# Kernel tuning notes

Measured on AMD Instinct MI355X. Metric: run time of the kernel, lower is better.

The kernel has to match this reference:

```python
import jax, jax.numpy as jnp
import numpy as np

WIN = 64
SHIFT = 32
HEADS = 12


def setup_inputs() -> dict:
    key = jax.random.key(0)
    ks = jax.random.split(key, 6)
    D = 768
    return {
        'x': jax.random.normal(ks[0], (16, 4096, D), dtype=jnp.float32),
        'qkv_w': jax.random.normal(ks[1], (3 * D, D), dtype=jnp.float32) * (D ** -0.5),
        'qkv_b': jax.random.normal(ks[2], (3 * D,), dtype=jnp.float32) * 0.02,
        'proj_w': jax.random.normal(ks[3], (D, D), dtype=jnp.float32) * (D ** -0.5),
        'proj_b': jax.random.normal(ks[4], (D,), dtype=jnp.float32) * 0.02,
        'rel_bias': jax.random.normal(ks[5], (HEADS, 2 * WIN - 1), dtype=jnp.float32) * 0.02,
    }


def reference(x, qkv_w, qkv_b, proj_w, proj_b, rel_bias):
    B, N, D = x.shape
    H, hd = HEADS, D // HEADS
    scale = hd ** -0.5
    if SHIFT:
        x = jnp.roll(x, SHIFT, axis=1)
    pad = (-N) % WIN
    if pad:
        x = jnp.pad(x, ((0, 0), (0, pad), (0, 0)))
    Np = x.shape[1]
    nW = Np // WIN
    # [B*nW, w, D] windows
    xw = x.reshape(B * nW, WIN, D)
    qkv = xw @ qkv_w.T + qkv_b                       # [B*nW, w, 3D]
    qkv = qkv.reshape(B * nW, WIN, 3, H, hd).transpose(2, 0, 3, 1, 4)
    q, k, v = qkv[0], qkv[1], qkv[2]                 # [B*nW, H, w, hd]
    attn = jnp.einsum('bhqd,bhkd->bhqk', q, k) * scale
    idx = jnp.arange(WIN)
    rel = idx[None, :] - idx[:, None] + (WIN - 1)    # [w, w] in [0, 2w-2]
    attn = attn + rel_bias[:, rel][None]             # gather bias per head
    attn = jax.nn.softmax(attn, axis=-1)
    y = jnp.einsum('bhqk,bhkd->bhqd', attn, v)       # [B*nW, H, w, hd]
    y = y.transpose(0, 2, 1, 3).reshape(B * nW, WIN, D)
    y = y @ proj_w.T + proj_b
    y = y.reshape(B, Np, D)
    if pad:
        y = y[:, :N, :]
    if SHIFT:
        y = jnp.roll(y, -SHIFT, axis=1)
    return y
```

## Files before the change

### kernel.cpp

```cpp
#include <hip/hip_runtime.h>
#include <hip/hip_bf16.h>
#include <stdint.h>

#define SEQ     4096
#define NBATCH  16
#define DMODEL  768
#define NHEAD   12
#define HDIM    64
#define WINSZ   64
#define SHIFT_T 32
#define QKV_N   (3*DMODEL)

typedef __attribute__((ext_vector_type(8))) short  bf16x8;
typedef __attribute__((ext_vector_type(4))) float  f32x4;

static __device__ __forceinline__ unsigned short f2bf(float f) {
  union { float f; unsigned u; } v; v.f = f;
  unsigned r = v.u + 0x7fffu + ((v.u >> 16) & 1u);
  return (unsigned short)(r >> 16);
}

__global__ void k_cvt_x(const float* __restrict__ x, unsigned short* __restrict__ xb,
                        long long c0, long long n8) {
  for (long long i = (long long)blockIdx.x*blockDim.x + threadIdx.x; i < n8;
       i += (long long)gridDim.x*blockDim.x) {
    long long e = i*8;
    int d = (int)(e % DMODEL);
    long long gt = c0 + e / DMODEL;
    int t = (int)(gt & (SEQ-1));
    long long b = gt >> 12;
    int ts = (t - SHIFT_T) & (SEQ-1);
    const float* src = x + (((b << 12) + ts) * (long long)DMODEL + d);
    float4 a0 = *(const float4*)src;
    float4 a1 = *(const float4*)(src + 4);
    bf16x8 o;
    o[0]=(short)f2bf(a0.x); o[1]=(short)f2bf(a0.y); o[2]=(short)f2bf(a0.z); o[3]=(short)f2bf(a0.w);
    o[4]=(short)f2bf(a1.x); o[5]=(short)f2bf(a1.y); o[6]=(short)f2bf(a1.z); o[7]=(short)f2bf(a1.w);
    *(bf16x8*)(xb + e) = o;
  }
}

__global__ void k_cvt_w(const float* __restrict__ w, unsigned short* __restrict__ wb, int n8) {
  int i = blockIdx.x*blockDim.x + threadIdx.x;
  if (i >= n8) return;
  float4 a0 = ((const float4*)w)[2*i];
  float4 a1 = ((const float4*)w)[2*i+1];
  bf16x8 o;
  o[0]=(short)f2bf(a0.x); o[1]=(short)f2bf(a0.y); o[2]=(short)f2bf(a0.z); o[3]=(short)f2bf(a0.w);
  o[4]=(short)f2bf(a1.x); o[5]=(short)f2bf(a1.y); o[6]=(short)f2bf(a1.z); o[7]=(short)f2bf(a1.w);
  ((bf16x8*)wb)[i] = o;
}

template<int MODE>
__global__ __launch_bounds__(256, 2)
void k_gemm_bt(const unsigned short* __restrict__ A, const unsigned short* __restrict__ Bw,
               const float* __restrict__ bias, unsigned short* __restrict__ Cb,
               float* __restrict__ Cf, int M, int N, int K, int nTN, long long c0) {
  __shared__ char sA[128*128];
  __shared__ char sB[128*128];
  int nwg = gridDim.x;
  int cpx = nwg >> 3;
  int wg  = (blockIdx.x & 7) * cpx + (blockIdx.x >> 3);
  int bm = wg / nTN, bn = wg % nTN;
  long long m0 = (long long)bm * 128;
  int n0 = bn * 128;
  int lane = threadIdx.x & 63, wid = threadIdx.x >> 6;
  int wr = wid >> 1, wc = wid & 1;
  int l8 = lane >> 3, lc = lane & 7;

  f32x4 acc[4][4];
  #pragma unroll
  for (int i = 0; i < 4; ++i)
    #pragma unroll
    for (int j = 0; j < 4; ++j) acc[i][j] = (f32x4){0.f,0.f,0.f,0.f};

  for (int kt = 0; kt < K; kt += 64) {
    __syncthreads();
    #pragma unroll
    for (int i = 0; i < 4; ++i) {
      int r   = i*4 + wid;
      int row = r*8 + l8;
      int ch  = lc ^ (row & 7);
      const unsigned short* ga = A  + (m0 + row) * (long long)K + kt + ch*8;
      const unsigned short* gb = Bw + (long long)(n0 + row) * K + kt + ch*8;
      __builtin_amdgcn_global_load_lds((const __attribute__((address_space(1))) unsigned int*)(const void*)ga,
          (__attribute__((address_space(3))) unsigned int*)(void*)(sA + r*1024), 16, 0, 0);
      __builtin_amdgcn_global_load_lds((const __attribute__((address_space(1))) unsigned int*)(const void*)gb,
          (__attribute__((address_space(3))) unsigned int*)(void*)(sB + r*1024), 16, 0, 0);
    }
    __syncthreads();
    #pragma unroll
    for (int kk = 0; kk < 2; ++kk) {
      bf16x8 af[4], bf[4];
      #pragma unroll
      for (int mf = 0; mf < 4; ++mf) {
        int row = wr*64 + mf*16 + (lane & 15);
        int p = row*128 + (kk*32 + (lane >> 4)*8)*2;
        af[mf] = *(const bf16x8*)(sA + (p ^ ((row & 7) << 4)));
      }
      #pragma unroll
      for (int nf = 0; nf < 4; ++nf) {
        int row = wc*64 + nf*16 + (lane & 15);
        int p = row*128 + (kk*32 + (lane >> 4)*8)*2;
        bf[nf] = *(const bf16x8*)(sB + (p ^ ((row & 7) << 4)));
      }
      #pragma unroll
      for (int mf = 0; mf < 4; ++mf)
        #pragma unroll
        for (int nf = 0; nf < 4; ++nf)
          acc[mf][nf] = __builtin_amdgcn_mfma_f32_16x16x32_bf16(af[mf], bf[nf], acc[mf][nf], 0, 0, 0);
    }
  }

  int cl = lane & 15, g4 = lane >> 4;
  #pragma unroll
  for (int mf = 0; mf < 4; ++mf) {
    #pragma unroll
    for (int nf = 0; nf < 4; ++nf) {
      int n = n0 + wc*64 + nf*16 + cl;
      float bv = bias[n];
      #pragma unroll
      for (int r = 0; r < 4; ++r) {
        long long m = m0 + wr*64 + mf*16 + g4*4 + r;
        float v = acc[mf][nf][r] + bv;
        if (MODE == 0) {
          Cb[m * (long long)N + n] = f2bf(v);
        } else {
          long long gm = c0 + m;
          long long om = (gm & ~(long long)(SEQ-1)) | ((gm - SHIFT_T) & (long long)(SEQ-1));
          Cf[om * (long long)N + n] = v;
        }
      }
    }
  }
}

__global__ __launch_bounds__(256, 4)
void k_attn(const unsigned short* __restrict__ qkv, const float* __restrict__ rel_bias,
            unsigned short* __restrict__ y) {
  int w = blockIdx.x / NHEAD;
  int h = blockIdx.x - w*NHEAD;
  __shared__ unsigned short sQ[64*72], sK[64*72], sV[64*72];
  __shared__ unsigned short sP[4][16*72];
  __shared__ float rb[128];
  int tid = threadIdx.x, lane = tid & 63, wid = tid >> 6;
  int cl = lane & 15, g4 = lane >> 4;

  if (tid < 2*WINSZ - 1) rb[tid] = rel_bias[h*(2*WINSZ-1) + tid];

  const unsigned short* base = qkv + (long long)w*WINSZ*QKV_N + h*HDIM;
  #pragma unroll
  for (int pass = 0; pass < 2; ++pass) {
    int row = (tid >> 3) + pass*32;
    int ch  = tid & 7;
    const unsigned short* src = base + (long long)row*QKV_N + ch*8;
    *(bf16x8*)(sQ + row*72 + ch*8) = *(const bf16x8*)(src);
    *(bf16x8*)(sK + row*72 + ch*8) = *(const bf16x8*)(src + DMODEL);
    *(bf16x8*)(sV + row*72 + ch*8) = *(const bf16x8*)(src + 2*DMODEL);
  }
  __syncthreads();

  f32x4 sc[4];
  #pragma unroll
  for (int nt = 0; nt < 4; ++nt) sc[nt] = (f32x4){0.f,0.f,0.f,0.f};
  #pragma unroll
  for (int kk = 0; kk < 2; ++kk) {
    bf16x8 aq = *(const bf16x8*)(sQ + (wid*16 + cl)*72 + kk*32 + g4*8);
    #pragma unroll
    for (int nt = 0; nt < 4; ++nt) {
      bf16x8 bk = *(const bf16x8*)(sK + (nt*16 + cl)*72 + kk*32 + g4*8);
      sc[nt] = __builtin_amdgcn_mfma_f32_16x16x32_bf16(aq, bk, sc[nt], 0, 0, 0);
    }
  }

  float pv[4][4];
  #pragma unroll
  for (int r = 0; r < 4; ++r) {
    int qi = wid*16 + g4*4 + r;
    float mx = -1e30f;
    #pragma unroll
    for (int nt = 0; nt < 4; ++nt) {
      int kj = nt*16 + cl;
      float v = sc[nt][r]*0.125f + rb[kj - qi + (WINSZ-1)];
      pv[nt][r] = v;
      mx = fmaxf(mx, v);
    }
    #pragma unroll
    for (int m = 1; m < 16; m <<= 1) mx = fmaxf(mx, __shfl_xor(mx, m, 64));
    float sum = 0.f;
    #pragma unroll
    for (int nt = 0; nt < 4; ++nt) { float e = __expf(pv[nt][r]-mx); pv[nt][r] = e; sum += e; }
    #pragma unroll
    for (int m = 1; m < 16; m <<= 1) sum += __shfl_xor(sum, m, 64);
    float inv = 1.f / sum;
    #pragma unroll
    for (int nt = 0; nt < 4; ++nt)
      sP[wid][(g4*4+r)*72 + nt*16 + cl] = f2bf(pv[nt][r]*inv);
  }

  f32x4 o[4];
  #pragma unroll
  for (int nt = 0; nt < 4; ++nt) o[nt] = (f32x4){0.f,0.f,0.f,0.f};
  #pragma unroll
  for (int kk = 0; kk < 2; ++kk) {
    bf16x8 ap = *(const bf16x8*)(&sP[wid][cl*72 + kk*32 + g4*8]);
    #pragma unroll
    for (int nt = 0; nt < 4; ++nt) {
      bf16x8 bv;
      #pragma unroll
      for (int j = 0; j < 8; ++j)
        bv[j] = (short)sV[(kk*32 + g4*8 + j)*72 + nt*16 + cl];
      o[nt] = __builtin_amdgcn_mfma_f32_16x16x32_bf16(ap, bv, o[nt], 0, 0, 0);
    }
  }

  long long tokbase = (long long)w * WINSZ;
  #pragma unroll
  for (int nt = 0; nt < 4; ++nt)
    #pragma unroll
    for (int r = 0; r < 4; ++r) {
      int row = wid*16 + g4*4 + r;
      y[(tokbase + row) * (long long)DMODEL + h*HDIM + nt*16 + cl] = f2bf(o[nt][r]);
    }
}

extern "C" void kernel_launch(void* const* d_in, const int* in_sizes, int n_in,
                              void* d_out, int out_size, void* d_ws, size_t ws_size,
                              hipStream_t stream) {
  const float* x      = (const float*)d_in[0];
  const float* qkv_w  = (const float*)d_in[1];
  const float* qkv_b  = (const float*)d_in[2];
  const float* proj_w = (const float*)d_in[3];
  const float* proj_b = (const float*)d_in[4];
  const float* rel_b  = (const float*)d_in[5];
  float* out = (float*)d_out;

  const long long NTOK = (long long)NBATCH * SEQ;
  const size_t wbytes = (size_t)QKV_N*DMODEL*2 + (size_t)DMODEL*DMODEL*2;

  int C = 16;
  for (int c : {1, 2, 4, 8, 16}) {
    size_t tpc = (size_t)NTOK / c;
    size_t need = tpc*QKV_N*2 + tpc*DMODEL*2 + wbytes;
    if (need <= ws_size) { C = c; break; }
  }
  long long tpc = NTOK / C;

  char* ws = (char*)d_ws;
  unsigned short* qkvb = (unsigned short*)ws;
  unsigned short* xb   = (unsigned short*)(ws + (size_t)tpc*QKV_N*2);
  unsigned short* wq   = (unsigned short*)(ws + (size_t)tpc*QKV_N*2 + (size_t)tpc*DMODEL*2);
  unsigned short* wp   = wq + (size_t)QKV_N*DMODEL;

  k_cvt_w<<<(QKV_N*DMODEL/8 + 255)/256, 256, 0, stream>>>(qkv_w, wq, QKV_N*DMODEL/8);
  k_cvt_w<<<(DMODEL*DMODEL/8 + 255)/256, 256, 0, stream>>>(proj_w, wp, DMODEL*DMODEL/8);

  for (int c = 0; c < C; ++c) {
    long long c0 = (long long)c * tpc;
    long long n8 = tpc * DMODEL / 8;
    int cvtGrid = (int)((n8 + 255) / 256); if (cvtGrid > 2048) cvtGrid = 2048;
    k_cvt_x<<<cvtGrid, 256, 0, stream>>>(x, xb, c0, n8);

    int mT = (int)(tpc / 128);
    k_gemm_bt<0><<<mT * (QKV_N/128), 256, 0, stream>>>(xb, wq, qkv_b, qkvb, nullptr,
                                                       (int)tpc, QKV_N, DMODEL, QKV_N/128, c0);
    k_attn<<<(int)(tpc/WINSZ) * NHEAD, 256, 0, stream>>>(qkvb, rel_b, xb );
    k_gemm_bt<1><<<mT * (DMODEL/128), 256, 0, stream>>>(xb, wp, proj_b, nullptr, out,
                                                        (int)tpc, DMODEL, DMODEL, DMODEL/128, c0);
  }
}
```

Measured before the change: 559.9 us.

## Replace GEMM with 256x256-tile, 8-wave, 4-stage LDS-pipelined kernel

```diff
diff --git a/kernel.cpp b/kernel.cpp
--- a/kernel.cpp
+++ b/kernel.cpp
@@ -19,6 +19,10 @@
   unsigned r = v.u + 0x7fffu + ((v.u >> 16) & 1u);
   return (unsigned short)(r >> 16);
 }
+
+#define G2L(gp, lp) __builtin_amdgcn_global_load_lds( \
+    (const __attribute__((address_space(1))) unsigned*)(const void*)(gp), \
+    (__attribute__((address_space(3))) unsigned*)(void*)(lp), 16, 0, 0)
 
 __global__ void k_cvt_x(const float* __restrict__ x, unsigned short* __restrict__ xb,
                         long long c0, long long n8) {
@@ -52,76 +56,127 @@
 }
 
 template<int MODE>
-__global__ __launch_bounds__(256, 2)
-void k_gemm_bt(const unsigned short* __restrict__ A, const unsigned short* __restrict__ Bw,
+__global__ __launch_bounds__(512, 1)
+void k_gemm256(const unsigned short* __restrict__ A, const unsigned short* __restrict__ Bw,
                const float* __restrict__ bias, unsigned short* __restrict__ Cb,
                float* __restrict__ Cf, int M, int N, int K, int nTN, long long c0) {
-  __shared__ char sA[128*128];
-  __shared__ char sB[128*128];
+  __shared__ char lds[4*32768];
+  const int nsl = K >> 5;
   int nwg = gridDim.x;
   int cpx = nwg >> 3;
   int wg  = (blockIdx.x & 7) * cpx + (blockIdx.x >> 3);
-  int bm = wg / nTN, bn = wg % nTN;
-  long long m0 = (long long)bm * 128;
-  int n0 = bn * 128;
-  int lane = threadIdx.x & 63, wid = threadIdx.x >> 6;
-  int wr = wid >> 1, wc = wid & 1;
-  int l8 = lane >> 3, lc = lane & 7;
-
-  f32x4 acc[4][4];
-  #pragma unroll
-  for (int i = 0; i < 4; ++i)
+  int bm = wg / nTN, bn = wg - bm*nTN;
+  long long m0 = (long long)bm * 256;
+  int n0 = bn * 256;
+  int tid = threadIdx.x;
+  int lane = tid & 63, wid = tid >> 6;
+  int wr = wid >> 2, wc = wid & 3;
+  int cl = lane & 15, g4 = lane >> 4;
+
+  const long long K2 = 2LL * K;
+  const char* gA0 = (const char*)A + (m0 + (tid >> 2)) * K2 + (tid & 3) * 16;
+  const char* gA1 = gA0 + 128 * K2;
+  const char* gB0 = (const char*)Bw + (long long)(n0 + (tid >> 2)) * K2 + (tid & 3) * 16;
+  const char* gB1 = gB0 + 128 * K2;
+  int ldst = tid * 16;
+
+  int aoff = (wr * 128 + cl) * 64 + g4 * 16;
+  int boff = 16384 + (wc * 64 + cl) * 64 + g4 * 16;
+
+  f32x4 acc[8][4];
+  #pragma unroll
+  for (int i = 0; i < 8; ++i)
     #pragma unroll
     for (int j = 0; j < 4; ++j) acc[i][j] = (f32x4){0.f,0.f,0.f,0.f};
 
-  for (int kt = 0; kt < K; kt += 64) {
-    __syncthreads();
-    #pragma unroll
-    for (int i = 0; i < 4; ++i) {
-      int r   = i*4 + wid;
-      int row = r*8 + l8;
-      int ch  = lc ^ (row & 7);
-      const unsigned short* ga = A  + (m0 + row) * (long long)K + kt + ch*8;
-      const unsigned short* gb = Bw + (long long)(n0 + row) * K + kt + ch*8;
-      __builtin_amdgcn_global_load_lds((const __attribute__((address_space(1))) unsigned int*)(const void*)ga,
-          (__attribute__((address_space(3))) unsigned int*)(void*)(sA + r*1024), 16, 0, 0);
-      __builtin_amdgcn_global_load_lds((const __attribute__((address_space(1))) unsigned int*)(const void*)gb,
-          (__attribute__((address_space(3))) unsigned int*)(void*)(sB + r*1024), 16, 0, 0);
-    }
-    __syncthreads();
-    #pragma unroll
-    for (int kk = 0; kk < 2; ++kk) {
-      bf16x8 af[4], bf[4];
-      #pragma unroll
-      for (int mf = 0; mf < 4; ++mf) {
-        int row = wr*64 + mf*16 + (lane & 15);
-        int p = row*128 + (kk*32 + (lane >> 4)*8)*2;
-        af[mf] = *(const bf16x8*)(sA + (p ^ ((row & 7) << 4)));
-      }
-      #pragma unroll
-      for (int nf = 0; nf < 4; ++nf) {
-        int row = wc*64 + nf*16 + (lane & 15);
-        int p = row*128 + (kk*32 + (lane >> 4)*8)*2;
-        bf[nf] = *(const bf16x8*)(sB + (p ^ ((row & 7) << 4)));
-      }
-      #pragma unroll
-      for (int mf = 0; mf < 4; ++mf)
-        #pragma unroll
-        for (int nf = 0; nf < 4; ++nf)
-          acc[mf][nf] = __builtin_amdgcn_mfma_f32_16x16x32_bf16(af[mf], bf[nf], acc[mf][nf], 0, 0, 0);
-    }
-  }
-
-  int cl = lane & 15, g4 = lane >> 4;
-  #pragma unroll
-  for (int mf = 0; mf < 4; ++mf) {
+  {
+    char* s0 = lds;
+    char* s1 = lds + 32768;
+    G2L(gA0,       s0 + ldst);
+    G2L(gA1,       s0 + 8192  + ldst);
+    G2L(gB0,       s0 + 16384 + ldst);
+    G2L(gB1,       s0 + 24576 + ldst);
+    G2L(gA0 + 64,  s1 + ldst);
+    G2L(gA1 + 64,  s1 + 8192  + ldst);
+    G2L(gB0 + 64,  s1 + 16384 + ldst);
+    G2L(gB1 + 64,  s1 + 24576 + ldst);
+    asm volatile("s_waitcnt vmcnt(4)" ::: "memory");
+    __builtin_amdgcn_sched_barrier(0);
+    __builtin_amdgcn_s_barrier();
+  }
+
+#define MFMA_ROW(av, m) \
+    acc[m][0] = __builtin_amdgcn_mfma_f32_16x16x32_bf16(av, b0, acc[m][0], 0, 0, 0); \
+    acc[m][1] = __builtin_amdgcn_mfma_f32_16x16x32_bf16(av, b1, acc[m][1], 0, 0, 0); \
+    acc[m][2] = __builtin_amdgcn_mfma_f32_16x16x32_bf16(av, b2, acc[m][2], 0, 0, 0); \
+    acc[m][3] = __builtin_amdgcn_mfma_f32_16x16x32_bf16(av, b3, acc[m][3], 0, 0, 0);
+
+  for (int s = 0; s < nsl; ++s) {
+    char* sb  = lds + ((s & 3) << 15);
+    char* stb = lds + (((s + 2) & 3) << 15);
+    long long kb2 = (long long)(s + 2) << 6;
+    bool doStage = (s + 2) < nsl;
+
+    bf16x8 a0 = *(const bf16x8*)(sb + aoff);
+    bf16x8 a1 = *(const bf16x8*)(sb + aoff + 1024);
+    bf16x8 a2 = *(const bf16x8*)(sb + aoff + 2048);
+    bf16x8 a3 = *(const bf16x8*)(sb + aoff + 3072);
+    bf16x8 b0 = *(const bf16x8*)(sb + boff);
+    bf16x8 b1 = *(const bf16x8*)(sb + boff + 1024);
+    bf16x8 b2 = *(const bf16x8*)(sb + boff + 2048);
+    bf16x8 b3 = *(const bf16x8*)(sb + boff + 3072);
+    if (doStage) {
+      G2L(gA0 + kb2, stb + ldst);
+      G2L(gA1 + kb2, stb + 8192 + ldst);
+    }
+    __builtin_amdgcn_sched_barrier(0);
+    __builtin_amdgcn_s_barrier();
+    asm volatile("s_waitcnt lgkmcnt(0)" ::: "memory");
+    __builtin_amdgcn_sched_barrier(0);
+    __builtin_amdgcn_s_setprio(1);
+    MFMA_ROW(a0, 0)
+    MFMA_ROW(a1, 1)
+    MFMA_ROW(a2, 2)
+    MFMA_ROW(a3, 3)
+    __builtin_amdgcn_s_setprio(0);
+    __builtin_amdgcn_sched_barrier(0);
+    __builtin_amdgcn_s_barrier();
+
+    bf16x8 a4 = *(const bf16x8*)(sb + aoff + 4096);
+    bf16x8 a5 = *(const bf16x8*)(sb + aoff + 5120);
+    bf16x8 a6 = *(const bf16x8*)(sb + aoff + 6144);
+    bf16x8 a7 = *(const bf16x8*)(sb + aoff + 7168);
+    if (doStage) {
+      G2L(gB0 + kb2, stb + 16384 + ldst);
+      G2L(gB1 + kb2, stb + 24576 + ldst);
+      asm volatile("s_waitcnt vmcnt(4)" ::: "memory");
+    } else if (s + 1 < nsl) {
+      asm volatile("s_waitcnt vmcnt(0)" ::: "memory");
+    }
+    __builtin_amdgcn_sched_barrier(0);
+    __builtin_amdgcn_s_barrier();
+    asm volatile("s_waitcnt lgkmcnt(0)" ::: "memory");
+    __builtin_amdgcn_sched_barrier(0);
+    __builtin_amdgcn_s_setprio(1);
+    MFMA_ROW(a4, 4)
+    MFMA_ROW(a5, 5)
+    MFMA_ROW(a6, 6)
+    MFMA_ROW(a7, 7)
+    __builtin_amdgcn_s_setprio(0);
+    __builtin_amdgcn_sched_barrier(0);
+    __builtin_amdgcn_s_barrier();
+  }
+#undef MFMA_ROW
+
+  #pragma unroll
+  for (int mf = 0; mf < 8; ++mf) {
     #pragma unroll
     for (int nf = 0; nf < 4; ++nf) {
       int n = n0 + wc*64 + nf*16 + cl;
       float bv = bias[n];
       #pragma unroll
       for (int r = 0; r < 4; ++r) {
-        long long m = m0 + wr*64 + mf*16 + g4*4 + r;
+        long long m = m0 + wr*128 + mf*16 + g4*4 + r;
         float v = acc[mf][nf][r] + bv;
         if (MODE == 0) {
           Cb[m * (long long)N + n] = f2bf(v);
@@ -261,11 +316,11 @@
     int cvtGrid = (int)((n8 + 255) / 256); if (cvtGrid > 2048) cvtGrid = 2048;
     k_cvt_x<<<cvtGrid, 256, 0, stream>>>(x, xb, c0, n8);
 
-    int mT = (int)(tpc / 128);
-    k_gemm_bt<0><<<mT * (QKV_N/128), 256, 0, stream>>>(xb, wq, qkv_b, qkvb, nullptr,
-                                                       (int)tpc, QKV_N, DMODEL, QKV_N/128, c0);
+    int mT = (int)(tpc / 256);
+    k_gemm256<0><<<mT * (QKV_N/256), 512, 0, stream>>>(xb, wq, qkv_b, qkvb, nullptr,
+                                                       (int)tpc, QKV_N, DMODEL, QKV_N/256, c0);
     k_attn<<<(int)(tpc/WINSZ) * NHEAD, 256, 0, stream>>>(qkvb, rel_b, xb );
-    k_gemm_bt<1><<<mT * (DMODEL/128), 256, 0, stream>>>(xb, wp, proj_b, nullptr, out,
-                                                        (int)tpc, DMODEL, DMODEL, DMODEL/128, c0);
-  }
-}
+    k_gemm256<1><<<mT * (DMODEL/256), 512, 0, stream>>>(xb, wp, proj_b, nullptr, out,
+                                                        (int)tpc, DMODEL, DMODEL, DMODEL/256, c0);
+  }
+}
```

Measured after the change: 534.4 us. 1.05x faster.

## Replace 128x128 GEMM with 256x256 double-buffered 8-wave pipelined GEMM

Applied to the files above, without the earlier changes.

```diff
diff --git a/kernel.cpp b/kernel.cpp
--- a/kernel.cpp
+++ b/kernel.cpp
@@ -11,14 +11,18 @@
 #define SHIFT_T 32
 #define QKV_N   (3*DMODEL)
 
-typedef __attribute__((ext_vector_type(8))) short  bf16x8;
-typedef __attribute__((ext_vector_type(4))) float  f32x4;
+typedef __attribute__((ext_vector_type(8)))  short bf16x8;
+typedef __attribute__((ext_vector_type(4)))  float f32x4;
 
 static __device__ __forceinline__ unsigned short f2bf(float f) {
   union { float f; unsigned u; } v; v.f = f;
   unsigned r = v.u + 0x7fffu + ((v.u >> 16) & 1u);
   return (unsigned short)(r >> 16);
 }
+
+#define G2L(gp, lp) __builtin_amdgcn_global_load_lds( \
+    (const __attribute__((address_space(1))) unsigned*)(const void*)(gp), \
+    (__attribute__((address_space(3))) unsigned*)(void*)(lp), 16, 0, 0)
 
 __global__ void k_cvt_x(const float* __restrict__ x, unsigned short* __restrict__ xb,
                         long long c0, long long n8) {
@@ -51,77 +55,146 @@
   ((bf16x8*)wb)[i] = o;
 }
 
+#define MFMA16(a,b,c) __builtin_amdgcn_mfma_f32_16x16x32_bf16(a,b,c,0,0,0)
+#define LDS8(p) (*(const bf16x8*)(p))
+
 template<int MODE>
-__global__ __launch_bounds__(256, 2)
-void k_gemm_bt(const unsigned short* __restrict__ A, const unsigned short* __restrict__ Bw,
+__global__ __launch_bounds__(512, 1)
+void k_gemm256(const unsigned short* __restrict__ A, const unsigned short* __restrict__ Bw,
                const float* __restrict__ bias, unsigned short* __restrict__ Cb,
                float* __restrict__ Cf, int M, int N, int K, int nTN, long long c0) {
-  __shared__ char sA[128*128];
-  __shared__ char sB[128*128];
+  __shared__ char lds[131072];
+  const int nt = K >> 6;
   int nwg = gridDim.x;
   int cpx = nwg >> 3;
   int wg  = (blockIdx.x & 7) * cpx + (blockIdx.x >> 3);
-  int bm = wg / nTN, bn = wg % nTN;
-  long long m0 = (long long)bm * 128;
-  int n0 = bn * 128;
-  int lane = threadIdx.x & 63, wid = threadIdx.x >> 6;
-  int wr = wid >> 1, wc = wid & 1;
-  int l8 = lane >> 3, lc = lane & 7;
-
-  f32x4 acc[4][4];
-  #pragma unroll
-  for (int i = 0; i < 4; ++i)
+  int bm = wg / nTN, bn = wg - bm*nTN;
+  long long m0 = (long long)bm * 256;
+  int n0 = bn * 256;
+  int tid = threadIdx.x;
+  int lane = tid & 63, wid = tid >> 6;
+  int wr = wid >> 2, wc = wid & 3;
+  int cl = lane & 15, g4 = lane >> 4;
+
+  const long long K2 = 2LL * K;
+  int L  = tid * 16;
+  int Ls = L ^ (((L >> 7) & 7) << 4);
+  int srow = Ls >> 7, scol = Ls & 127;
+  const char* gAr0 = (const char*)A + (m0 +       srow) * K2 + scol;
+  const char* gAr1 = (const char*)A + (m0 +  64 + srow) * K2 + scol;
+  const char* gAr2 = (const char*)A + (m0 + 128 + srow) * K2 + scol;
+  const char* gAr3 = (const char*)A + (m0 + 192 + srow) * K2 + scol;
+  const char* gBr0 = (const char*)Bw + (long long)(n0 +       srow) * K2 + scol;
+  const char* gBr1 = (const char*)Bw + (long long)(n0 +  64 + srow) * K2 + scol;
+  const char* gBr2 = (const char*)Bw + (long long)(n0 + 128 + srow) * K2 + scol;
+  const char* gBr3 = (const char*)Bw + (long long)(n0 + 192 + srow) * K2 + scol;
+
+  int p0 = cl*128 + ((g4*16) ^ ((cl & 7) << 4));
+  int p1 = p0 ^ 64;
+  int RA0 = wr*16384;
+  int RA1 = wr*16384 + 8192;
+  int BB  = 32768 + wc*8192;
+
+  f32x4 acc[8][4];
+  #pragma unroll
+  for (int i = 0; i < 8; ++i)
     #pragma unroll
     for (int j = 0; j < 4; ++j) acc[i][j] = (f32x4){0.f,0.f,0.f,0.f};
 
-  for (int kt = 0; kt < K; kt += 64) {
-    __syncthreads();
-    #pragma unroll
-    for (int i = 0; i < 4; ++i) {
-      int r   = i*4 + wid;
-      int row = r*8 + l8;
-      int ch  = lc ^ (row & 7);
-      const unsigned short* ga = A  + (m0 + row) * (long long)K + kt + ch*8;
-      const unsigned short* gb = Bw + (long long)(n0 + row) * K + kt + ch*8;
-      __builtin_amdgcn_global_load_lds((const __attribute__((address_space(1))) unsigned int*)(const void*)ga,
-          (__attribute__((address_space(3))) unsigned int*)(void*)(sA + r*1024), 16, 0, 0);
-      __builtin_amdgcn_global_load_lds((const __attribute__((address_space(1))) unsigned int*)(const void*)gb,
-          (__attribute__((address_space(3))) unsigned int*)(void*)(sB + r*1024), 16, 0, 0);
-    }
-    __syncthreads();
-    #pragma unroll
-    for (int kk = 0; kk < 2; ++kk) {
-      bf16x8 af[4], bf[4];
-      #pragma unroll
-      for (int mf = 0; mf < 4; ++mf) {
-        int row = wr*64 + mf*16 + (lane & 15);
-        int p = row*128 + (kk*32 + (lane >> 4)*8)*2;
-        af[mf] = *(const bf16x8*)(sA + (p ^ ((row & 7) << 4)));
-      }
-      #pragma unroll
-      for (int nf = 0; nf < 4; ++nf) {
-        int row = wc*64 + nf*16 + (lane & 15);
-        int p = row*128 + (kk*32 + (lane >> 4)*8)*2;
-        bf[nf] = *(const bf16x8*)(sB + (p ^ ((row & 7) << 4)));
-      }
-      #pragma unroll
-      for (int mf = 0; mf < 4; ++mf)
-        #pragma unroll
-        for (int nf = 0; nf < 4; ++nf)
-          acc[mf][nf] = __builtin_amdgcn_mfma_f32_16x16x32_bf16(af[mf], bf[nf], acc[mf][nf], 0, 0, 0);
-    }
-  }
-
-  int cl = lane & 15, g4 = lane >> 4;
-  #pragma unroll
-  for (int mf = 0; mf < 4; ++mf) {
+#define MMPH(MA, MB, x0, x1, y0, y1) \
+  acc[MA][0]=MFMA16(x0,b00,acc[MA][0]); acc[MA][1]=MFMA16(x0,b10,acc[MA][1]); \
+  acc[MA][2]=MFMA16(x0,b20,acc[MA][2]); acc[MA][3]=MFMA16(x0,b30,acc[MA][3]); \
+  acc[MB][0]=MFMA16(y0,b00,acc[MB][0]); acc[MB][1]=MFMA16(y0,b10,acc[MB][1]); \
+  acc[MB][2]=MFMA16(y0,b20,acc[MB][2]); acc[MB][3]=MFMA16(y0,b30,acc[MB][3]); \
+  acc[MA][0]=MFMA16(x1,b01,acc[MA][0]); acc[MA][1]=MFMA16(x1,b11,acc[MA][1]); \
+  acc[MA][2]=MFMA16(x1,b21,acc[MA][2]); acc[MA][3]=MFMA16(x1,b31,acc[MA][3]); \
+  acc[MB][0]=MFMA16(y1,b01,acc[MB][0]); acc[MB][1]=MFMA16(y1,b11,acc[MB][1]); \
+  acc[MB][2]=MFMA16(y1,b21,acc[MB][2]); acc[MB][3]=MFMA16(y1,b31,acc[MB][3]);
+
+#define BARR __builtin_amdgcn_s_barrier()
+#define SBAR __builtin_amdgcn_sched_barrier(0)
+#define LGK0 do { asm volatile("s_waitcnt lgkmcnt(0)" ::: "memory"); SBAR; } while(0)
+
+#define TILE(RD, ST, DOSTAGE, WBSTR, DOWA) do {                               \
+    const char* rb = (RD); char* stb = (ST);                                  \
+    bf16x8 b00,b01,b10,b11,b20,b21,b30,b31;                                   \
+    {                              \
+      bf16x8 x0 = LDS8(rb + RA0        + p0), x1 = LDS8(rb + RA0        + p1);\
+      bf16x8 y0 = LDS8(rb + RA0 + 2048 + p0), y1 = LDS8(rb + RA0 + 2048 + p1);\
+      b00 = LDS8(rb + BB        + p0);  b01 = LDS8(rb + BB        + p1);      \
+      b10 = LDS8(rb + BB + 2048 + p0);  b11 = LDS8(rb + BB + 2048 + p1);      \
+      b20 = LDS8(rb + BB + 4096 + p0);  b21 = LDS8(rb + BB + 4096 + p1);      \
+      b30 = LDS8(rb + BB + 6144 + p0);  b31 = LDS8(rb + BB + 6144 + p1);      \
+      if (DOSTAGE) { G2L(gBr0, stb + 32768 + L); G2L(gBr1, stb + 40960 + L); }\
+      asm volatile("s_waitcnt lgkmcnt(8)" ::: "memory"); SBAR;                \
+      BARR; LGK0;                                                             \
+      __builtin_amdgcn_s_setprio(1);                                          \
+      MMPH(0, 1, x0, x1, y0, y1)                                              \
+      __builtin_amdgcn_s_setprio(0); SBAR; BARR;                              \
+    }                                                                         \
+    {              \
+      bf16x8 x0 = LDS8(rb + RA0 + 4096 + p0), x1 = LDS8(rb + RA0 + 4096 + p1);\
+      bf16x8 y0 = LDS8(rb + RA0 + 6144 + p0), y1 = LDS8(rb + RA0 + 6144 + p1);\
+      if (DOSTAGE) { G2L(gBr2, stb + 49152 + L); G2L(gBr3, stb + 57344 + L); }\
+      SBAR; BARR; LGK0;                                                       \
+      __builtin_amdgcn_s_setprio(1);                                          \
+      MMPH(2, 3, x0, x1, y0, y1)                                              \
+      __builtin_amdgcn_s_setprio(0); SBAR;                                    \
+      asm volatile(WBSTR ::: "memory"); SBAR; BARR;                           \
+    }                                                                         \
+    {                                      \
+      bf16x8 x0 = LDS8(rb + RA1        + p0), x1 = LDS8(rb + RA1        + p1);\
+      bf16x8 y0 = LDS8(rb + RA1 + 2048 + p0), y1 = LDS8(rb + RA1 + 2048 + p1);\
+      if (DOSTAGE) { G2L(gAr0, stb + L); G2L(gAr2, stb + 16384 + L); }        \
+      SBAR; BARR; LGK0;                                                       \
+      __builtin_amdgcn_s_setprio(1);                                          \
+      MMPH(4, 5, x0, x1, y0, y1)                                              \
+      __builtin_amdgcn_s_setprio(0); SBAR; BARR;                              \
+    }                                                                         \
+    {        \
+      bf16x8 x0 = LDS8(rb + RA1 + 4096 + p0), x1 = LDS8(rb + RA1 + 4096 + p1);\
+      bf16x8 y0 = LDS8(rb + RA1 + 6144 + p0), y1 = LDS8(rb + RA1 + 6144 + p1);\
+      if (DOSTAGE) { G2L(gAr1, stb + 8192 + L); G2L(gAr3, stb + 24576 + L);   \
+                     gAr0 += 128; gAr1 += 128; gAr2 += 128; gAr3 += 128;      \
+                     gBr0 += 128; gBr1 += 128; gBr2 += 128; gBr3 += 128; }    \
+      SBAR; BARR; LGK0;                                                       \
+      __builtin_amdgcn_s_setprio(1);                                          \
+      MMPH(6, 7, x0, x1, y0, y1)                                              \
+      __builtin_amdgcn_s_setprio(0); SBAR;                                    \
+      if (DOWA) { asm volatile("s_waitcnt vmcnt(2)" ::: "memory"); }          \
+      SBAR; BARR;                                                             \
+    }                                                                         \
+  } while (0)
+
+  G2L(gBr0, lds + 32768 + L); G2L(gBr1, lds + 40960 + L);
+  G2L(gBr2, lds + 49152 + L); G2L(gBr3, lds + 57344 + L);
+  G2L(gAr0, lds + L);         G2L(gAr2, lds + 16384 + L);
+  G2L(gAr1, lds + 8192 + L);  G2L(gAr3, lds + 24576 + L);
+  gAr0 += 128; gAr1 += 128; gAr2 += 128; gAr3 += 128;
+  gBr0 += 128; gBr1 += 128; gBr2 += 128; gBr3 += 128;
+  asm volatile("s_waitcnt vmcnt(2)" ::: "memory");
+  SBAR; BARR;
+
+  char* const bufA = lds;
+  char* const bufB = lds + 65536;
+  for (int i = 0; i < (nt - 2) / 2; ++i) {
+    TILE(bufA, bufB, 1, "s_waitcnt vmcnt(4)", 1);
+    TILE(bufB, bufA, 1, "s_waitcnt vmcnt(4)", 1);
+  }
+  TILE(bufA, bufB, 1, "s_waitcnt vmcnt(4)", 1);
+  TILE(bufB, bufA, 0, "s_waitcnt vmcnt(0)", 0);
+#undef TILE
+#undef MMPH
+
+  #pragma unroll
+  for (int mf = 0; mf < 8; ++mf) {
     #pragma unroll
     for (int nf = 0; nf < 4; ++nf) {
       int n = n0 + wc*64 + nf*16 + cl;
       float bv = bias[n];
       #pragma unroll
       for (int r = 0; r < 4; ++r) {
-        long long m = m0 + wr*64 + mf*16 + g4*4 + r;
+        long long m = m0 + wr*128 + mf*16 + g4*4 + r;
         float v = acc[mf][nf][r] + bv;
         if (MODE == 0) {
           Cb[m * (long long)N + n] = f2bf(v);
@@ -261,11 +334,11 @@
     int cvtGrid = (int)((n8 + 255) / 256); if (cvtGrid > 2048) cvtGrid = 2048;
     k_cvt_x<<<cvtGrid, 256, 0, stream>>>(x, xb, c0, n8);
 
-    int mT = (int)(tpc / 128);
-    k_gemm_bt<0><<<mT * (QKV_N/128), 256, 0, stream>>>(xb, wq, qkv_b, qkvb, nullptr,
-                                                       (int)tpc, QKV_N, DMODEL, QKV_N/128, c0);
+    int mT = (int)(tpc / 256);
+    k_gemm256<0><<<mT * (QKV_N/256), 512, 0, stream>>>(xb, wq, qkv_b, qkvb, nullptr,
+                                                       (int)tpc, QKV_N, DMODEL, QKV_N/256, c0);
     k_attn<<<(int)(tpc/WINSZ) * NHEAD, 256, 0, stream>>>(qkvb, rel_b, xb );
-    k_gemm_bt<1><<<mT * (DMODEL/128), 256, 0, stream>>>(xb, wp, proj_b, nullptr, out,
-                                                        (int)tpc, DMODEL, DMODEL, DMODEL/128, c0);
-  }
-}
+    k_gemm256<1><<<mT * (DMODEL/256), 512, 0, stream>>>(xb, wp, proj_b, nullptr, out,
+                                                        (int)tpc, DMODEL, DMODEL, DMODEL/256, c0);
+  }
+}
```

Result: faster. 503.3 us (-10.1%).
